# Performance work log

Hardware: AMD Instinct MI355X
Metric: run time of the kernel (lower is better)

Reference implementation:

```python
import jax, jax.numpy as jnp
import numpy as np

N = 50000
E = 800000
D = 128


def _gcn_layer(x, row, col, ew, W, b, n):
    # PyG GCNConv (normalize=True, add_self_loops=True):
    # self-loops were already appended to row/col/ew by the caller.
    deg = jax.ops.segment_sum(ew, col, num_segments=n)          # [N]
    dis = jnp.where(deg > 0, jax.lax.rsqrt(jnp.maximum(deg, 1e-12)), 0.0)
    norm = dis[row] * ew * dis[col]                              # [E+N]
    h = x @ W                                                    # [N, D]
    msg = h[row] * norm[:, None]                                 # [E+N, D] gather-scale
    out = jax.ops.segment_sum(msg, col, num_segments=n)          # scatter-add
    return out + b


def setup_inputs() -> dict:
    key = jax.random.key(0)
    k1, k2, k3, k4, k5 = jax.random.split(key, 5)
    x = jax.random.normal(k1, (N, D), dtype=jnp.float32)
    edge_index = jax.random.randint(k2, (2, E), 0, N, dtype=jnp.int64)
    edge_weight = jax.random.uniform(k3, (E,), dtype=jnp.float32)
    s = 1.0 / np.sqrt(D)
    W1 = jax.random.uniform(k4, (D, D), minval=-s, maxval=s, dtype=jnp.float32)
    b1 = jnp.zeros((D,), dtype=jnp.float32)
    W2 = jax.random.uniform(k5, (D, D), minval=-s, maxval=s, dtype=jnp.float32)
    b2 = jnp.zeros((D,), dtype=jnp.float32)
    return {"x": x, "edge_index": edge_index, "edge_weight": edge_weight,
            "W1": W1, "b1": b1, "W2": W2, "b2": b2}


def reference(x, edge_index, edge_weight, W1, b1, W2, b2):
    n = x.shape[0]
    loop = jnp.arange(n, dtype=edge_index.dtype)
    row = jnp.concatenate([edge_index[0], loop])
    col = jnp.concatenate([edge_index[1], loop])
    ew = jnp.concatenate([edge_weight, jnp.ones((n,), dtype=edge_weight.dtype)])
    h = _gcn_layer(x, row, col, ew, W1, b1, n)
    h = jax.nn.relu(h)
    # F.dropout(training=self.training): identity in eval mode
    out = _gcn_layer(h, row, col, ew, W2, b2, n)
    return out
```

## Files before the change

kernel.cpp:

```cpp
#include <hip/hip_runtime.h>

#define NN 50000
#define NE 800000
#define DD 128

#define CAP 64
#define QPAD 8
#define FIX_SCALE 16777216.0f
#define LOW40 ((1ULL << 40) - 1)
#define NWELEM 16384
#define GEMM_GRID ((NN + 127) / 128)
#define PLACE_GRID ((NE + 255) / 256)

typedef __attribute__((ext_vector_type(8))) short short8;
typedef __attribute__((ext_vector_type(4))) float floatx4;
typedef __attribute__((ext_vector_type(4))) _Float16 half4;
typedef __attribute__((ext_vector_type(8))) _Float16 half8;


__device__ __forceinline__ void split_trunc(float x, short& hi, short& lo) {
    unsigned uh = __float_as_uint(x) >> 16;
    hi = (short)uh;
    float r = x - __uint_as_float(uh << 16);
    lo = (short)(__float_as_uint(r) >> 16);
}


__global__ void init_prep(unsigned long long* __restrict__ cursor64,
                          const float* __restrict__ W1, const float* __restrict__ W2,
                          unsigned short* __restrict__ w1hi, unsigned short* __restrict__ w1lo,
                          unsigned short* __restrict__ w2hi, unsigned short* __restrict__ w2lo) {
    int t = blockIdx.x * blockDim.x + threadIdx.x;
    if (t < NN) cursor64[t * QPAD] = 0ULL;
    int u = t - NN;
    if (u >= 0 && u < 2 * NWELEM) {
        int which = u >> 14;
        int idx = u & (NWELEM - 1);
        int k = idx >> 7, n = idx & 127;
        const float* W = which ? W2 : W1;
        unsigned short* whi = which ? w2hi : w1hi;
        unsigned short* wlo = which ? w2lo : w1lo;
        short h, l;
        split_trunc(W[idx], h, l);
        whi[n * DD + k] = (unsigned short)h;
        wlo[n * DD + k] = (unsigned short)l;
    }
}


template <bool RELU, bool SCALE, typename InT>
__device__ __forceinline__ void gemm_core(int bid, const InT* __restrict__ in,
                                          const unsigned short* __restrict__ whi,
                                          const unsigned short* __restrict__ wlo,
                                          const float* __restrict__ dis,
                                          _Float16* __restrict__ out) {
    int lane = threadIdx.x & 63;
    int wid = threadIdx.x >> 6;
    int cg = wid & 1;
    int rg = wid >> 1;
    int l16 = lane & 15;
    int quad = lane >> 4;
    int koff_base = quad * 8;

    short8 bhi[4][4], blo[4][4];
#pragma unroll
    for (int t = 0; t < 4; t++) {
        int n = cg * 64 + t * 16 + l16;
#pragma unroll
        for (int ks = 0; ks < 4; ks++) {
            int koff = ks * 32 + koff_base;
            bhi[t][ks] = *(const short8*)(whi + n * DD + koff);
            blo[t][ks] = *(const short8*)(wlo + n * DD + koff);
        }
    }

#pragma unroll
    for (int chunk = 0; chunk < 4; chunk++) {
        int base = bid * 128 + chunk * 32 + rg * 16;
        int m = base + l16;
        int mld = (m < NN) ? m : 0;
        const InT* xr = in + (size_t)mld * DD;

        short8 ahi[4], alo[4];
#pragma unroll
        for (int ks = 0; ks < 4; ks++) {
            int koff = ks * 32 + koff_base;
            float v[8];
            if constexpr (sizeof(InT) == 4) {
                float4 a0 = *(const float4*)(xr + koff);
                float4 a1 = *(const float4*)(xr + koff + 4);
                v[0] = a0.x; v[1] = a0.y; v[2] = a0.z; v[3] = a0.w;
                v[4] = a1.x; v[5] = a1.y; v[6] = a1.z; v[7] = a1.w;
            } else {
                half8 a = *(const half8*)(xr + koff);
#pragma unroll
                for (int j = 0; j < 8; j++) v[j] = (float)a[j];
            }
#pragma unroll
            for (int j = 0; j < 8; j++) {
                float xv = RELU ? fmaxf(v[j], 0.0f) : v[j];
                short h, l;
                split_trunc(xv, h, l);
                ahi[ks][j] = h;
                alo[ks][j] = l;
            }
        }

        floatx4 acc[4];
#pragma unroll
        for (int t = 0; t < 4; t++) acc[t] = (floatx4)(0.0f);

#pragma unroll
        for (int ks = 0; ks < 4; ks++) {
#pragma unroll
            for (int t = 0; t < 4; t++) {
                acc[t] = __builtin_amdgcn_mfma_f32_16x16x32_bf16(ahi[ks], bhi[t][ks], acc[t], 0, 0, 0);
                acc[t] = __builtin_amdgcn_mfma_f32_16x16x32_bf16(alo[ks], bhi[t][ks], acc[t], 0, 0, 0);
                acc[t] = __builtin_amdgcn_mfma_f32_16x16x32_bf16(ahi[ks], blo[t][ks], acc[t], 0, 0, 0);
            }
        }

#pragma unroll
        for (int r = 0; r < 4; r++) {
            int rowm = base + quad * 4 + r;
            if (rowm < NN) {
                float dsc = SCALE ? dis[rowm] : 1.0f;
                _Float16* o = out + (size_t)rowm * DD + cg * 64 + l16;
#pragma unroll
                for (int t = 0; t < 4; t++) o[t * 16] = (_Float16)(acc[t][r] * dsc);
            }
        }
    }
}


__device__ __forceinline__ void place_core(int e, const int* __restrict__ row,
                                           const int* __restrict__ col,
                                           const float* __restrict__ ew,
                                           unsigned long long* __restrict__ cursor64,
                                           uint2* __restrict__ epk) {
    if (e >= NE) return;
    int c = col[e];
    float w = ew[e];
    unsigned q = (unsigned)(w * FIX_SCALE + 0.5f);
    unsigned long long old = atomicAdd(&cursor64[c * QPAD], (1ULL << 40) | (unsigned long long)q);
    int rank = min((int)(old >> 40), CAP - 1);
    uint2 p;
    p.x = (unsigned)(row[e] * DD);
    p.y = __float_as_uint(w);
    epk[(c << 6) + rank] = p;
}


__global__ __launch_bounds__(256) void gemm1_place(const float* __restrict__ x,
                                                   const unsigned short* __restrict__ w1hi,
                                                   const unsigned short* __restrict__ w1lo,
                                                   _Float16* __restrict__ g,
                                                   const int* __restrict__ row,
                                                   const int* __restrict__ col,
                                                   const float* __restrict__ ew,
                                                   unsigned long long* __restrict__ cursor64,
                                                   uint2* __restrict__ epk) {
    if (blockIdx.x < GEMM_GRID) {
        gemm_core<false, false, float>(blockIdx.x, x, w1hi, w1lo, nullptr, g);
    } else {
        int e = (blockIdx.x - GEMM_GRID) * 256 + threadIdx.x;
        place_core(e, row, col, ew, cursor64, epk);
    }
}

__global__ __launch_bounds__(256, 2) void gemm2(const _Float16* __restrict__ in,
                                                const unsigned short* __restrict__ whi,
                                                const unsigned short* __restrict__ wlo,
                                                const float* __restrict__ dis,
                                                _Float16* __restrict__ out) {
    gemm_core<true, true, _Float16>(blockIdx.x, in, whi, wlo, dis, out);
}


__global__ __launch_bounds__(256) void node_dis_scale(const unsigned long long* __restrict__ cursor64,
                                                      float* __restrict__ dis,
                                                      int* __restrict__ endarr,
                                                      _Float16* __restrict__ g) {
    int t = blockIdx.x * blockDim.x + threadIdx.x;
    int i = t >> 4, sub = t & 15;
    if (i >= NN) return;
    unsigned long long cv = cursor64[i * QPAD];
    float deg = 1.0f + (float)(cv & LOW40) * (1.0f / FIX_SCALE);
    float d = rsqrtf(deg);
    if (sub == 0) {
        dis[i] = d;
        endarr[i] = (i << 6) + min((int)(cv >> 40), CAP);
    }
    half8* gp = (half8*)(g + (size_t)i * DD + sub * 8);
    half8 v = *gp;
#pragma unroll
    for (int j = 0; j < 8; j++) v[j] = (_Float16)((float)v[j] * d);
    *gp = v;
}


template <typename OutT>
__global__ __launch_bounds__(256) void agg_half(const int* __restrict__ endarr,
                                                const uint2* __restrict__ epk,
                                                const _Float16* __restrict__ g,
                                                const float* __restrict__ dis,
                                                const float* __restrict__ bias,
                                                OutT* __restrict__ out) {
    int i = (blockIdx.x * blockDim.x + threadIdx.x) >> 6;
    int lane = threadIdx.x & 63;
    int s = lane & 31;
    int half = lane >> 5;
    if (i >= NN) return;

    half4 gv = *(const half4*)(g + (size_t)i * DD + s * 4);
    float4 bb = ((const float4*)bias)[s];
    float d = dis[i];

    float ax = 0.0f, ay = 0.0f, az = 0.0f, aw = 0.0f;

    int start = i << 6;
    int end = endarr[i];
    int j = start + half;
    for (; j + 6 < end; j += 8) {
        uint2 p0 = epk[j], p1 = epk[j + 2], p2 = epk[j + 4], p3 = epk[j + 6];
        half4 v0 = *(const half4*)(g + p0.x + s * 4);
        half4 v1 = *(const half4*)(g + p1.x + s * 4);
        half4 v2 = *(const half4*)(g + p2.x + s * 4);
        half4 v3 = *(const half4*)(g + p3.x + s * 4);
        float n0 = __uint_as_float(p0.y), n1 = __uint_as_float(p1.y);
        float n2 = __uint_as_float(p2.y), n3 = __uint_as_float(p3.y);
        ax = fmaf(n0, (float)v0.x, ax); ay = fmaf(n0, (float)v0.y, ay);
        az = fmaf(n0, (float)v0.z, az); aw = fmaf(n0, (float)v0.w, aw);
        ax = fmaf(n1, (float)v1.x, ax); ay = fmaf(n1, (float)v1.y, ay);
        az = fmaf(n1, (float)v1.z, az); aw = fmaf(n1, (float)v1.w, aw);
        ax = fmaf(n2, (float)v2.x, ax); ay = fmaf(n2, (float)v2.y, ay);
        az = fmaf(n2, (float)v2.z, az); aw = fmaf(n2, (float)v2.w, aw);
        ax = fmaf(n3, (float)v3.x, ax); ay = fmaf(n3, (float)v3.y, ay);
        az = fmaf(n3, (float)v3.z, az); aw = fmaf(n3, (float)v3.w, aw);
    }
    for (; j < end; j += 2) {
        uint2 p = epk[j];
        float nm = __uint_as_float(p.y);
        half4 v = *(const half4*)(g + p.x + s * 4);
        ax = fmaf(nm, (float)v.x, ax); ay = fmaf(nm, (float)v.y, ay);
        az = fmaf(nm, (float)v.z, az); aw = fmaf(nm, (float)v.w, aw);
    }

    ax += __shfl_xor(ax, 32);
    ay += __shfl_xor(ay, 32);
    az += __shfl_xor(az, 32);
    aw += __shfl_xor(aw, 32);

    if (half == 0) {
        float ox = bb.x + d * (ax + (float)gv.x);
        float oy = bb.y + d * (ay + (float)gv.y);
        float oz = bb.z + d * (az + (float)gv.z);
        float ow = bb.w + d * (aw + (float)gv.w);
        if constexpr (sizeof(OutT) == 2) {
            half4 o;
            o.x = (_Float16)ox; o.y = (_Float16)oy;
            o.z = (_Float16)oz; o.w = (_Float16)ow;
            *(half4*)(out + (size_t)i * DD + s * 4) = o;
        } else {
            float4 o;
            o.x = ox; o.y = oy; o.z = oz; o.w = ow;
            ((float4*)(out + (size_t)i * DD))[s] = o;
        }
    }
}


extern "C" void kernel_launch(void* const* d_in, const int* in_sizes, int n_in,
                              void* d_out, int out_size, void* d_ws, size_t ws_size,
                              hipStream_t stream) {
    const float* x  = (const float*)d_in[0];
    const int*   ei = (const int*)d_in[1];
    const float* ew = (const float*)d_in[2];
    const float* W1 = (const float*)d_in[3];
    const float* b1 = (const float*)d_in[4];
    const float* W2 = (const float*)d_in[5];
    const float* b2 = (const float*)d_in[6];
    float* out = (float*)d_out;

    float* ws      = (float*)d_ws;
    float* dis     = ws;
    int*   endarr  = (int*)(ws + 50000);
    unsigned long long* cursor64 = (unsigned long long*)(ws + 100000);
    uint2* epk     = (uint2*)(ws + 900000);
    _Float16* gbuf = (_Float16*)(ws + 7300000);
    unsigned short* wt1hi = (unsigned short*)(ws + 10500000);
    unsigned short* wt1lo = (unsigned short*)(ws + 10508192);
    unsigned short* wt2hi = (unsigned short*)(ws + 10516384);
    unsigned short* wt2lo = (unsigned short*)(ws + 10524576);
    _Float16* out1 = (_Float16*)(ws + 10532768);

    const int* rowi = ei;
    const int* coli = ei + NE;

    init_prep<<<(NN + 2 * NWELEM + 255) / 256, 256, 0, stream>>>(
        cursor64, W1, W2, wt1hi, wt1lo, wt2hi, wt2lo);

    gemm1_place<<<GEMM_GRID + PLACE_GRID, 256, 0, stream>>>(
        x, wt1hi, wt1lo, gbuf, rowi, coli, ew, cursor64, epk);

    node_dis_scale<<<(NN * 16) / 256, 256, 0, stream>>>(cursor64, dis, endarr, gbuf);

    const int agg_grid = (NN * 64) / 256 + 1;

    agg_half<_Float16><<<agg_grid, 256, 0, stream>>>(endarr, epk, gbuf, dis, b1, out1);

    gemm2<<<GEMM_GRID, 256, 0, stream>>>(out1, wt2hi, wt2lo, dis, gbuf);

    agg_half<float><<<agg_grid, 256, 0, stream>>>(endarr, epk, gbuf, dis, b2, out);
}
```

Baseline: 231.2 us.

## Fold source-degree scaling into layer-1 aggregation and emit pre-split bf16 activations

Removes the separate pass that scaled the layer-1 GEMM output by dis per node. Layer-1 aggregation now multiplies each edge weight by dis of the source node (an extra gather per edge) and applies dis to the self term. The same kernel also applies ReLU and writes the output as bf16 hi/lo pairs, so gemm2 loads split operands directly instead of converting and splitting fp16 input. The cost is more per-edge dis loads and twice the intermediate bytes (hi+lo u16 in place of one fp16).

New measurement: 242.0 us. +4.7%, slower.

```diff
diff --git a/kernel.cpp b/kernel.cpp
--- a/kernel.cpp
+++ b/kernel.cpp
@@ -16,6 +16,7 @@
 typedef __attribute__((ext_vector_type(4))) float floatx4;
 typedef __attribute__((ext_vector_type(4))) _Float16 half4;
 typedef __attribute__((ext_vector_type(8))) _Float16 half8;
+typedef __attribute__((ext_vector_type(4))) unsigned short ushort4v;
 
 
 __device__ __forceinline__ void split_trunc(float x, short& hi, short& lo) {
@@ -48,8 +49,10 @@
 }
 
 
-template <bool RELU, bool SCALE, typename InT>
+template <bool RELU, bool SCALE, bool SPLITIN, typename InT>
 __device__ __forceinline__ void gemm_core(int bid, const InT* __restrict__ in,
+                                          const unsigned short* __restrict__ inHi,
+                                          const unsigned short* __restrict__ inLo,
                                           const unsigned short* __restrict__ whi,
                                           const unsigned short* __restrict__ wlo,
                                           const float* __restrict__ dis,
@@ -79,30 +82,35 @@
         int base = bid * 128 + chunk * 32 + rg * 16;
         int m = base + l16;
         int mld = (m < NN) ? m : 0;
-        const InT* xr = in + (size_t)mld * DD;
 
         short8 ahi[4], alo[4];
 #pragma unroll
         for (int ks = 0; ks < 4; ks++) {
             int koff = ks * 32 + koff_base;
-            float v[8];
-            if constexpr (sizeof(InT) == 4) {
-                float4 a0 = *(const float4*)(xr + koff);
-                float4 a1 = *(const float4*)(xr + koff + 4);
-                v[0] = a0.x; v[1] = a0.y; v[2] = a0.z; v[3] = a0.w;
-                v[4] = a1.x; v[5] = a1.y; v[6] = a1.z; v[7] = a1.w;
+            if constexpr (SPLITIN) {
+                ahi[ks] = *(const short8*)(inHi + (size_t)mld * DD + koff);
+                alo[ks] = *(const short8*)(inLo + (size_t)mld * DD + koff);
             } else {
-                half8 a = *(const half8*)(xr + koff);
-#pragma unroll
-                for (int j = 0; j < 8; j++) v[j] = (float)a[j];
-            }
-#pragma unroll
-            for (int j = 0; j < 8; j++) {
-                float xv = RELU ? fmaxf(v[j], 0.0f) : v[j];
-                short h, l;
-                split_trunc(xv, h, l);
-                ahi[ks][j] = h;
-                alo[ks][j] = l;
+                const InT* xr = in + (size_t)mld * DD;
+                float v[8];
+                if constexpr (sizeof(InT) == 4) {
+                    float4 a0 = *(const float4*)(xr + koff);
+                    float4 a1 = *(const float4*)(xr + koff + 4);
+                    v[0] = a0.x; v[1] = a0.y; v[2] = a0.z; v[3] = a0.w;
+                    v[4] = a1.x; v[5] = a1.y; v[6] = a1.z; v[7] = a1.w;
+                } else {
+                    half8 a = *(const half8*)(xr + koff);
+#pragma unroll
+                    for (int j = 0; j < 8; j++) v[j] = (float)a[j];
+                }
+#pragma unroll
+                for (int j = 0; j < 8; j++) {
+                    float xv = RELU ? fmaxf(v[j], 0.0f) : v[j];
+                    short h, l;
+                    split_trunc(xv, h, l);
+                    ahi[ks][j] = h;
+                    alo[ks][j] = l;
+                }
             }
         }
 
@@ -162,51 +170,46 @@
                                                    unsigned long long* __restrict__ cursor64,
                                                    uint2* __restrict__ epk) {
     if (blockIdx.x < GEMM_GRID) {
-        gemm_core<false, false, float>(blockIdx.x, x, w1hi, w1lo, nullptr, g);
+        gemm_core<false, false, false, float>(blockIdx.x, x, nullptr, nullptr,
+                                              w1hi, w1lo, nullptr, g);
     } else {
         int e = (blockIdx.x - GEMM_GRID) * 256 + threadIdx.x;
         place_core(e, row, col, ew, cursor64, epk);
     }
 }
 
-__global__ __launch_bounds__(256, 2) void gemm2(const _Float16* __restrict__ in,
+__global__ __launch_bounds__(256, 2) void gemm2(const unsigned short* __restrict__ o1hi,
+                                                const unsigned short* __restrict__ o1lo,
                                                 const unsigned short* __restrict__ whi,
                                                 const unsigned short* __restrict__ wlo,
                                                 const float* __restrict__ dis,
                                                 _Float16* __restrict__ out) {
-    gemm_core<true, true, _Float16>(blockIdx.x, in, whi, wlo, dis, out);
-}
-
-
-__global__ __launch_bounds__(256) void node_dis_scale(const unsigned long long* __restrict__ cursor64,
-                                                      float* __restrict__ dis,
-                                                      int* __restrict__ endarr,
-                                                      _Float16* __restrict__ g) {
-    int t = blockIdx.x * blockDim.x + threadIdx.x;
-    int i = t >> 4, sub = t & 15;
+    gemm_core<false, true, true, _Float16>(blockIdx.x, (const _Float16*)nullptr, o1hi, o1lo,
+                                           whi, wlo, dis, out);
+}
+
+
+__global__ __launch_bounds__(256) void node_dis(const unsigned long long* __restrict__ cursor64,
+                                                float* __restrict__ dis,
+                                                int* __restrict__ endarr) {
+    int i = blockIdx.x * blockDim.x + threadIdx.x;
     if (i >= NN) return;
     unsigned long long cv = cursor64[i * QPAD];
     float deg = 1.0f + (float)(cv & LOW40) * (1.0f / FIX_SCALE);
-    float d = rsqrtf(deg);
-    if (sub == 0) {
-        dis[i] = d;
-        endarr[i] = (i << 6) + min((int)(cv >> 40), CAP);
-    }
-    half8* gp = (half8*)(g + (size_t)i * DD + sub * 8);
-    half8 v = *gp;
-#pragma unroll
-    for (int j = 0; j < 8; j++) v[j] = (_Float16)((float)v[j] * d);
-    *gp = v;
-}
-
-
-template <typename OutT>
+    dis[i] = rsqrtf(deg);
+    endarr[i] = (i << 6) + min((int)(cv >> 40), CAP);
+}
+
+
+template <int MODE>
 __global__ __launch_bounds__(256) void agg_half(const int* __restrict__ endarr,
                                                 const uint2* __restrict__ epk,
                                                 const _Float16* __restrict__ g,
                                                 const float* __restrict__ dis,
                                                 const float* __restrict__ bias,
-                                                OutT* __restrict__ out) {
+                                                float* __restrict__ outf,
+                                                unsigned short* __restrict__ ohi,
+                                                unsigned short* __restrict__ olo) {
     int i = (blockIdx.x * blockDim.x + threadIdx.x) >> 6;
     int lane = threadIdx.x & 63;
     int s = lane & 31;
@@ -230,6 +233,10 @@
         half4 v3 = *(const half4*)(g + p3.x + s * 4);
         float n0 = __uint_as_float(p0.y), n1 = __uint_as_float(p1.y);
         float n2 = __uint_as_float(p2.y), n3 = __uint_as_float(p3.y);
+        if constexpr (MODE == 0) {
+            n0 *= dis[p0.x >> 7]; n1 *= dis[p1.x >> 7];
+            n2 *= dis[p2.x >> 7]; n3 *= dis[p3.x >> 7];
+        }
         ax = fmaf(n0, (float)v0.x, ax); ay = fmaf(n0, (float)v0.y, ay);
         az = fmaf(n0, (float)v0.z, az); aw = fmaf(n0, (float)v0.w, aw);
         ax = fmaf(n1, (float)v1.x, ax); ay = fmaf(n1, (float)v1.y, ay);
@@ -242,6 +249,7 @@
     for (; j < end; j += 2) {
         uint2 p = epk[j];
         float nm = __uint_as_float(p.y);
+        if constexpr (MODE == 0) nm *= dis[p.x >> 7];
         half4 v = *(const half4*)(g + p.x + s * 4);
         ax = fmaf(nm, (float)v.x, ax); ay = fmaf(nm, (float)v.y, ay);
         az = fmaf(nm, (float)v.z, az); aw = fmaf(nm, (float)v.w, aw);
@@ -253,19 +261,30 @@
     aw += __shfl_xor(aw, 32);
 
     if (half == 0) {
-        float ox = bb.x + d * (ax + (float)gv.x);
-        float oy = bb.y + d * (ay + (float)gv.y);
-        float oz = bb.z + d * (az + (float)gv.z);
-        float ow = bb.w + d * (aw + (float)gv.w);
-        if constexpr (sizeof(OutT) == 2) {
-            half4 o;
-            o.x = (_Float16)ox; o.y = (_Float16)oy;
-            o.z = (_Float16)oz; o.w = (_Float16)ow;
-            *(half4*)(out + (size_t)i * DD + s * 4) = o;
+        if constexpr (MODE == 0) {
+            float ox = bb.x + d * (ax + d * (float)gv.x);
+            float oy = bb.y + d * (ay + d * (float)gv.y);
+            float oz = bb.z + d * (az + d * (float)gv.z);
+            float ow = bb.w + d * (aw + d * (float)gv.w);
+            ox = fmaxf(ox, 0.0f); oy = fmaxf(oy, 0.0f);
+            oz = fmaxf(oz, 0.0f); ow = fmaxf(ow, 0.0f);
+            short hx, lx, hy, ly, hz, lz, hw, lw;
+            split_trunc(ox, hx, lx); split_trunc(oy, hy, ly);
+            split_trunc(oz, hz, lz); split_trunc(ow, hw, lw);
+            ushort4v vh, vl;
+            vh.x = (unsigned short)hx; vh.y = (unsigned short)hy;
+            vh.z = (unsigned short)hz; vh.w = (unsigned short)hw;
+            vl.x = (unsigned short)lx; vl.y = (unsigned short)ly;
+            vl.z = (unsigned short)lz; vl.w = (unsigned short)lw;
+            *(ushort4v*)(ohi + (size_t)i * DD + s * 4) = vh;
+            *(ushort4v*)(olo + (size_t)i * DD + s * 4) = vl;
         } else {
             float4 o;
-            o.x = ox; o.y = oy; o.z = oz; o.w = ow;
-            ((float4*)(out + (size_t)i * DD))[s] = o;
+            o.x = bb.x + d * (ax + (float)gv.x);
+            o.y = bb.y + d * (ay + (float)gv.y);
+            o.z = bb.z + d * (az + (float)gv.z);
+            o.w = bb.w + d * (aw + (float)gv.w);
+            ((float4*)(outf + (size_t)i * DD))[s] = o;
         }
     }
 }
@@ -293,7 +312,8 @@
     unsigned short* wt1lo = (unsigned short*)(ws + 10508192);
     unsigned short* wt2hi = (unsigned short*)(ws + 10516384);
     unsigned short* wt2lo = (unsigned short*)(ws + 10524576);
-    _Float16* out1 = (_Float16*)(ws + 10532768);
+    unsigned short* o1hi  = (unsigned short*)(ws + 10532768);
+    unsigned short* o1lo  = (unsigned short*)(ws + 13732768);
 
     const int* rowi = ei;
     const int* coli = ei + NE;
@@ -304,13 +324,15 @@
     gemm1_place<<<GEMM_GRID + PLACE_GRID, 256, 0, stream>>>(
         x, wt1hi, wt1lo, gbuf, rowi, coli, ew, cursor64, epk);
 
-    node_dis_scale<<<(NN * 16) / 256, 256, 0, stream>>>(cursor64, dis, endarr, gbuf);
+    node_dis<<<(NN + 255) / 256, 256, 0, stream>>>(cursor64, dis, endarr);
 
     const int agg_grid = (NN * 64) / 256 + 1;
 
-    agg_half<_Float16><<<agg_grid, 256, 0, stream>>>(endarr, epk, gbuf, dis, b1, out1);
-
-    gemm2<<<GEMM_GRID, 256, 0, stream>>>(out1, wt2hi, wt2lo, dis, gbuf);
-
-    agg_half<float><<<agg_grid, 256, 0, stream>>>(endarr, epk, gbuf, dis, b2, out);
-}
+    agg_half<0><<<agg_grid, 256, 0, stream>>>(endarr, epk, gbuf, dis, b1,
+                                              nullptr, o1hi, o1lo);
+
+    gemm2<<<GEMM_GRID, 256, 0, stream>>>(o1hi, o1lo, wt2hi, wt2lo, dis, gbuf);
+
+    agg_half<1><<<agg_grid, 256, 0, stream>>>(endarr, epk, gbuf, dis, b2,
+                                              out, nullptr, nullptr);
+}
```
